# Performance work log

Hardware: AMD Instinct MI355X
Metric: run time of the kernel (lower is better)

The kernel has to match this reference:

```python
import jax, jax.numpy as jnp
import numpy as np

B, L, C_IN, H, W = 4, 5, 64, 256, 128
QUERY_SIZE, KEY_SIZE = 32, 256


def _conv_relu(x, w, b, stride):
    # conv2DBatchNormRelu with BN (eval) folded into conv weights/bias
    y = jax.lax.conv_general_dilated(x, w, (stride, stride), [(1, 1), (1, 1)],
                                     dimension_numbers=('NCHW', 'OIHW', 'NCHW'))
    return jax.nn.relu(y + b[None, :, None, None])


def _policy_net(x, w1, b1, w2, b2, w3, b3):
    # policy_net4: three stride-2 4x4 conv blocks -> (N, 64, H/8, W/8)
    x = _conv_relu(x, w1, b1, 2)
    x = _conv_relu(x, w2, b2, 2)
    return _conv_relu(x, w3, b3, 2)


def _km_generator(feat, f1w, f1b, f2w, f2b, f3w, f3b):
    # km_generator_v2: global avg pool + MLP 64->256->128->out_size
    x = feat.mean(axis=(2, 3))
    x = jax.nn.relu(x @ f1w.T + f1b)
    x = jax.nn.relu(x @ f2w.T + f2b)
    return x @ f3w.T + f3b


def _affine_grid(theta, h, w):
    # torch F.affine_grid, align_corners=False
    xs = (jnp.arange(w, dtype=jnp.float32) + 0.5) * (2.0 / w) - 1.0
    ys = (jnp.arange(h, dtype=jnp.float32) + 0.5) * (2.0 / h) - 1.0
    gy, gx = jnp.meshgrid(ys, xs, indexing='ij')
    base = jnp.stack([gx, gy, jnp.ones_like(gx)], axis=-1)  # (h, w, 3)
    return jnp.einsum('nij,hwj->nhwi', theta, base)  # (N, h, w, 2)


def _grid_sample(img, grid):
    # torch F.grid_sample, bilinear, padding_mode='zeros', align_corners=False
    n, c, h, w = img.shape
    x = ((grid[..., 0] + 1.0) * w - 1.0) * 0.5
    y = ((grid[..., 1] + 1.0) * h - 1.0) * 0.5
    x0, y0 = jnp.floor(x), jnp.floor(y)

    def gather(ix, iy):
        valid = (ix >= 0) & (ix < w) & (iy >= 0) & (iy < h)
        ixc = jnp.clip(ix, 0, w - 1).astype(jnp.int32)
        iyc = jnp.clip(iy, 0, h - 1).astype(jnp.int32)
        vals = jax.vmap(lambda im, yy, xx: im[:, yy, xx])(img, iyc, ixc)  # (n, c, h, w)
        return vals * valid[:, None, :, :].astype(img.dtype)

    wx1 = (x - x0)[:, None]
    wx0 = 1.0 - wx1
    wy1 = (y - y0)[:, None]
    wy0 = 1.0 - wy1
    return (gather(x0, y0) * wx0 * wy0 + gather(x0 + 1.0, y0) * wx1 * wy0 +
            gather(x0, y0 + 1.0) * wx0 * wy1 + gather(x0 + 1.0, y0 + 1.0) * wx1 * wy1)


def setup_inputs() -> dict:
    key = jax.random.key(0)
    ks = jax.random.split(key, 24)
    s = 0.05
    eye = jnp.array([[1.0, 0.0, 0.0], [0.0, 1.0, 0.0]], jnp.float32)
    nam = jnp.broadcast_to(eye, (B, L, L, 2, 3)) + s * jax.random.normal(ks[1], (B, L, L, 2, 3), jnp.float32)
    return {
        'x': jax.random.normal(ks[0], (B * L, C_IN, H, W), jnp.float32),
        'record_len': jnp.full((B,), L, jnp.int32),
        'normalized_affine_matrix': nam,
        'conv_w1': s * jax.random.normal(ks[2], (32, C_IN, 4, 4), jnp.float32),
        'conv_b1': jnp.zeros((32,), jnp.float32),
        'conv_w2': s * jax.random.normal(ks[3], (64, 32, 4, 4), jnp.float32),
        'conv_b2': jnp.zeros((64,), jnp.float32),
        'conv_w3': s * jax.random.normal(ks[4], (64, 64, 4, 4), jnp.float32),
        'conv_b3': jnp.zeros((64,), jnp.float32),
        'key_f1w': s * jax.random.normal(ks[5], (256, 64), jnp.float32),
        'key_f1b': jnp.zeros((256,), jnp.float32),
        'key_f2w': s * jax.random.normal(ks[6], (128, 256), jnp.float32),
        'key_f2b': jnp.zeros((128,), jnp.float32),
        'key_f3w': s * jax.random.normal(ks[7], (KEY_SIZE, 128), jnp.float32),
        'key_f3b': jnp.zeros((KEY_SIZE,), jnp.float32),
        'qry_f1w': s * jax.random.normal(ks[8], (256, 64), jnp.float32),
        'qry_f1b': jnp.zeros((256,), jnp.float32),
        'qry_f2w': s * jax.random.normal(ks[9], (128, 256), jnp.float32),
        'qry_f2b': jnp.zeros((128,), jnp.float32),
        'qry_f3w': s * jax.random.normal(ks[10], (QUERY_SIZE, 128), jnp.float32),
        'qry_f3b': jnp.zeros((QUERY_SIZE,), jnp.float32),
        'attn_w': s * jax.random.normal(ks[11], (KEY_SIZE, QUERY_SIZE), jnp.float32),
        'attn_b': jnp.zeros((KEY_SIZE,), jnp.float32),
    }


def reference(x, record_len, normalized_affine_matrix,
              conv_w1, conv_b1, conv_w2, conv_b2, conv_w3, conv_b3,
              key_f1w, key_f1b, key_f2w, key_f2b, key_f3w, key_f3b,
              qry_f1w, qry_f1b, qry_f2w, qry_f2b, qry_f3w, qry_f3b,
              attn_w, attn_b):
    # record_len is constant (= L for every sample) -> static regroup as reshape
    xb = x.reshape(B, L, C_IN, H, W)
    tmats = normalized_affine_matrix[:, 0]  # t_matrix[0]: warp every cav to ego, (B, L, 2, 3)

    def fuse_one(xi, ti):
        neigh = _grid_sample(xi, _affine_grid(ti, H, W))  # (L, C, H, W)
        maps = _policy_net(neigh, conv_w1, conv_b1, conv_w2, conv_b2, conv_w3, conv_b3)
        keys = _km_generator(maps, key_f1w, key_f1b, key_f2w, key_f2b, key_f3w, key_f3b)  # (L, KEY)
        qry = _km_generator(maps[:1], qry_f1w, qry_f1b, qry_f2w, qry_f2b, qry_f3w, qry_f3b)  # (1, QUERY)
        q = qry @ attn_w.T + attn_b  # (1, KEY)
        attn = jax.nn.softmax(keys @ q[0])  # softmax over key/agent axis, (L,)
        return jnp.einsum('n,nchw->chw', attn, neigh)

    return jax.vmap(fuse_one)(xb, tmats)  # (B, C, H, W)
```

## Files before the change

### kernel.cpp

```cpp
#include <hip/hip_runtime.h>
#include <hip/hip_bf16.h>

typedef __attribute__((ext_vector_type(8))) short short8;
typedef __attribute__((ext_vector_type(8))) unsigned short ushort8;
typedef __attribute__((ext_vector_type(4))) float floatx4;

static __device__ __forceinline__ float bf2f(unsigned short h) {
    unsigned int u = ((unsigned int)h) << 16;
    float f;
    __builtin_memcpy(&f, &u, 4);
    return f;
}
static __device__ __forceinline__ unsigned short f2bf(float f) {
    unsigned int u;
    __builtin_memcpy(&u, &f, 4);
    u = (u + 0x7FFFu + ((u >> 16) & 1u)) >> 16;
    return (unsigned short)u;
}

#define P_NAM 0
#define P_B1 600
#define P_B2 632
#define P_B3 696
#define P_K1W 760
#define P_K1B 17144
#define P_K2W 17400
#define P_K2B 50168
#define P_K3W 50296
#define P_K3B 83064
#define P_Q1W 83320
#define P_Q1B 99704
#define P_Q2W 99960
#define P_Q2B 132728
#define P_Q3W 132856
#define P_Q3B 136952
#define P_AW 136984
#define P_AB 145176
#define P_TOTAL 145432

__global__ void k_detect(const unsigned short* __restrict__ x, int* __restrict__ flag) {
    const int lane = threadIdx.x;
    const unsigned short h = x[2 * lane];
    const int e = (h >> 7) & 0xFF;
    const int ok = (e >= 110 && e <= 140) ? 1 : 0;
    unsigned long long m = __ballot(ok);
    if (lane == 0) *flag = (__popcll(m) >= 48) ? 0 : 1;
}

struct ParamDesc {
    const void* src[18];
    int len[18];
    int dst[18];
};

__global__ __launch_bounds__(256) void k_convert(ParamDesc pd, const int* __restrict__ flag,
                                                 float* __restrict__ out) {
    int idx = blockIdx.x * 256 + threadIdx.x;
    const int isf = *flag;
    for (int t = 0; t < 18; ++t) {
        const int l = pd.len[t];
        if (idx < l) {
            float v = isf ? ((const float*)pd.src[t])[idx]
                          : bf2f(((const unsigned short*)pd.src[t])[idx]);
            out[pd.dst[t] + idx] = v;
            return;
        }
        idx -= l;
    }
}

__global__ __launch_bounds__(256) void k_pack(
    const void* __restrict__ w1, const void* __restrict__ w2, const void* __restrict__ w3,
    const int* __restrict__ flag, short* __restrict__ blobs)
{
    const int idx = blockIdx.x * 256 + threadIdx.x;
    const int isf = *flag;
    if (idx < 32768) {
        int j = idx & 7, lane = (idx >> 3) & 63, t = (idx >> 9) & 1,
            s = (idx >> 10) & 3, c = (idx >> 12) & 1, ky = (idx >> 13) & 3;
        int kp = s * 32 + (lane >> 4) * 8 + j;
        int kx = kp >> 5, ic = c * 32 + (kp & 31), oc = t * 16 + (lane & 15);
        int si = oc * 1024 + ic * 16 + ky * 4 + kx;
        float v = isf ? ((const float*)w1)[si] : bf2f(((const unsigned short*)w1)[si]);
        blobs[idx] = (short)f2bf(v);
    } else if (idx < 65536) {
        int i2 = idx - 32768;
        int j = i2 & 7, lane = (i2 >> 3) & 63, t = (i2 >> 9) & 3,
            s = (i2 >> 11) & 3, ky = (i2 >> 13) & 3;
        int kp = s * 32 + (lane >> 4) * 8 + j;
        int kx = kp >> 5, ic = kp & 31, oc = t * 16 + (lane & 15);
        int si = oc * 512 + ic * 16 + ky * 4 + kx;
        float v = isf ? ((const float*)w2)[si] : bf2f(((const unsigned short*)w2)[si]);
        blobs[idx] = (short)f2bf(v);
    } else if (idx < 131072) {
        int i3 = idx - 65536;
        int j = i3 & 7, lane = (i3 >> 3) & 63, t = (i3 >> 9) & 3,
            s = (i3 >> 11) & 3, c = (i3 >> 13) & 1, ky = (i3 >> 14) & 3;
        int kp = s * 32 + (lane >> 4) * 8 + j;
        int kx = kp >> 5, ic = c * 32 + (kp & 31), oc = t * 16 + (lane & 15);
        int si = oc * 1024 + ic * 16 + ky * 4 + kx;
        float v = isf ? ((const float*)w3)[si] : bf2f(((const unsigned short*)w3)[si]);
        blobs[idx] = (short)f2bf(v);
    }
}

__global__ __launch_bounds__(128) void k_gridsample(
    const void* __restrict__ xv,
    const float* __restrict__ P,
    const int* __restrict__ flag,
    unsigned short* __restrict__ neighCL)
{
    __shared__ unsigned int s_t32[128 * 33];
    unsigned short* s_t = (unsigned short*)s_t32;
    const int n = blockIdx.x;
    const int h = blockIdx.y;
    const int w = threadIdx.x;
    const int b = n / 5, l = n - b * 5;
    const float* th = P + P_NAM + (b * 25 + l) * 6;
    const float t00 = th[0], t01 = th[1], t02 = th[2];
    const float t10 = th[3], t11 = th[4], t12 = th[5];

    const float gxn = ((float)w + 0.5f) * (2.0f / 128.0f) - 1.0f;
    const float gyn = ((float)h + 0.5f) * (2.0f / 256.0f) - 1.0f;
    const float gx = t00 * gxn + t01 * gyn + t02;
    const float gy = t10 * gxn + t11 * gyn + t12;
    const float xs = ((gx + 1.0f) * 128.0f - 1.0f) * 0.5f;
    const float ys = ((gy + 1.0f) * 256.0f - 1.0f) * 0.5f;
    const float x0f = floorf(xs), y0f = floorf(ys);
    const int ix0 = (int)x0f, iy0 = (int)y0f;
    const int ix1 = ix0 + 1, iy1 = iy0 + 1;
    const float wx1 = xs - x0f, wx0 = 1.0f - wx1;
    const float wy1 = ys - y0f, wy0 = 1.0f - wy1;

    const float mx0 = (ix0 >= 0 && ix0 < 128) ? 1.0f : 0.0f;
    const float mx1 = (ix1 >= 0 && ix1 < 128) ? 1.0f : 0.0f;
    const float my0 = (iy0 >= 0 && iy0 < 256) ? 1.0f : 0.0f;
    const float my1 = (iy1 >= 0 && iy1 < 256) ? 1.0f : 0.0f;
    const int cx0 = min(max(ix0, 0), 127), cx1 = min(max(ix1, 0), 127);
    const int cy0 = min(max(iy0, 0), 255), cy1 = min(max(iy1, 0), 255);

    const float w00 = mx0 * my0 * wx0 * wy0, w10 = mx1 * my0 * wx1 * wy0;
    const float w01 = mx0 * my1 * wx0 * wy1, w11 = mx1 * my1 * wx1 * wy1;
    const int o00 = cy0 * 128 + cx0, o10 = cy0 * 128 + cx1;
    const int o01 = cy1 * 128 + cx0, o11 = cy1 * 128 + cx1;

    if (*flag) {
        const float* img = ((const float*)xv) + (size_t)n * 64 * 32768;
        for (int c = 0; c < 64; ++c) {
            const float* ic = img + c * 32768;
            const float r = ic[o00] * w00 + ic[o10] * w10 + ic[o01] * w01 + ic[o11] * w11;
            s_t[w * 66 + c] = f2bf(r);
        }
    } else {
        const unsigned short* img = ((const unsigned short*)xv) + (size_t)n * 64 * 32768;
        for (int c = 0; c < 64; ++c) {
            const unsigned short* ic = img + c * 32768;
            const float r = bf2f(ic[o00]) * w00 + bf2f(ic[o10]) * w10 +
                            bf2f(ic[o01]) * w01 + bf2f(ic[o11]) * w11;
            s_t[w * 66 + c] = f2bf(r);
        }
    }
    __syncthreads();
    unsigned int* gout = (unsigned int*)(neighCL + ((size_t)n * 32768 + (size_t)h * 128) * 64);
    for (int e = w; e < 4096; e += 128) {
        const int px = e >> 5, part = e & 31;
        gout[px * 32 + part] = s_t32[px * 33 + part];
    }
}

#define ROWSTR 1096

__global__ __launch_bounds__(128) void k_conv1m(
    const unsigned short* __restrict__ in, const short* __restrict__ blob1,
    const float* __restrict__ P, unsigned short* __restrict__ out)
{
    __shared__ unsigned short s_a[18 * ROWSTR];
    __shared__ float sb[32];
    const int n = blockIdx.x;
    const int oy0 = blockIdx.y * 8;
    const int ox0 = blockIdx.z * 16;
    const int tid = threadIdx.x;
    const int wv = tid >> 6, lane = tid & 63;
    const int ln = lane & 15, q = lane >> 4;
    const int mrow = ln >> 2, mcol = ln & 3;
    const int iny0 = 2 * oy0 - 1, inx0 = 2 * ox0 - 1;
    if (tid < 32) sb[tid] = P[P_B1 + tid];

    floatx4 acc[4][2];
#pragma unroll
    for (int f = 0; f < 4; ++f)
#pragma unroll
        for (int t = 0; t < 2; ++t) acc[f][t] = (floatx4)0.0f;

    const ushort8 z8 = (ushort8)0;
    for (int c = 0; c < 2; ++c) {
        __syncthreads();
        for (int e = tid; e < 2448; e += 128) {
            const int row = e / 136, rem = e - row * 136;
            const int col = rem >> 2, part = rem & 3;
            const int gy = iny0 + row, gxp = inx0 + col;
            ushort8 v = z8;
            if (gy >= 0 && gy < 256 && gxp >= 0 && gxp < 128)
                v = *(const ushort8*)(in + (((size_t)n * 32768 + gy * 128 + gxp) * 64 + c * 32 + part * 8));
            *(ushort8*)(s_a + row * ROWSTR + col * 32 + part * 8) = v;
        }
        __syncthreads();
#pragma unroll
        for (int ky = 0; ky < 4; ++ky) {
            short8 bfr[4][2];
            const short* bb = blob1 + ((ky * 2 + c) * 8) * 512 + lane * 8;
#pragma unroll
            for (int s = 0; s < 4; ++s)
#pragma unroll
                for (int t = 0; t < 2; ++t)
                    bfr[s][t] = *(const short8*)(bb + (s * 2 + t) * 512);
#pragma unroll
            for (int f = 0; f < 4; ++f) {
                const int base = (2 * ((f >> 1) * 4 + mrow) + ky) * ROWSTR +
                                 (wv * 8 + (f & 1) * 4 + mcol) * 64 + q * 8;
#pragma unroll
                for (int s = 0; s < 4; ++s) {
                    const short8 a = *(const short8*)(s_a + base + s * 32);
#pragma unroll
                    for (int t = 0; t < 2; ++t)
                        acc[f][t] = __builtin_amdgcn_mfma_f32_16x16x32_bf16(a, bfr[s][t], acc[f][t], 0, 0, 0);
                }
            }
        }
    }
#pragma unroll
    for (int f = 0; f < 4; ++f)
#pragma unroll
        for (int t = 0; t < 2; ++t)
#pragma unroll
            for (int r = 0; r < 4; ++r) {
                const int oc = t * 16 + ln;
                const int oy = oy0 + (f >> 1) * 4 + q;
                const int ox = ox0 + wv * 8 + (f & 1) * 4 + r;
                float v = acc[f][t][r] + sb[oc];
                v = v > 0.0f ? v : 0.0f;
                out[(((size_t)n * 128 + oy) * 64 + ox) * 32 + oc] = f2bf(v);
            }
}

__global__ __launch_bounds__(256) void k_conv2m(
    const unsigned short* __restrict__ in, const short* __restrict__ blob2,
    const float* __restrict__ P, unsigned short* __restrict__ out)
{
    __shared__ unsigned short s_a[18 * ROWSTR];
    __shared__ float sb[64];
    const int n = blockIdx.x;
    const int oy0 = blockIdx.y * 8;
    const int ox0 = blockIdx.z * 16;
    const int tid = threadIdx.x;
    const int wave = tid >> 6, lane = tid & 63;
    const int wcol = wave & 1, wt = wave >> 1;
    const int ln = lane & 15, q = lane >> 4;
    const int mrow = ln >> 2, mcol = ln & 3;
    const int iny0 = 2 * oy0 - 1, inx0 = 2 * ox0 - 1;
    if (tid < 64) sb[tid] = P[P_B2 + tid];

    floatx4 acc[4][2];
#pragma unroll
    for (int f = 0; f < 4; ++f)
#pragma unroll
        for (int t = 0; t < 2; ++t) acc[f][t] = (floatx4)0.0f;

    const ushort8 z8 = (ushort8)0;
    for (int e = tid; e < 2448; e += 256) {
        const int row = e / 136, rem = e - row * 136;
        const int col = rem >> 2, part = rem & 3;
        const int gy = iny0 + row, gxp = inx0 + col;
        ushort8 v = z8;
        if (gy >= 0 && gy < 128 && gxp >= 0 && gxp < 64)
            v = *(const ushort8*)(in + (((size_t)n * 8192 + gy * 64 + gxp) * 32 + part * 8));
        *(ushort8*)(s_a + row * ROWSTR + col * 32 + part * 8) = v;
    }
    __syncthreads();
#pragma unroll
    for (int ky = 0; ky < 4; ++ky) {
        short8 bfr[4][2];
#pragma unroll
        for (int s = 0; s < 4; ++s)
#pragma unroll
            for (int tt = 0; tt < 2; ++tt)
                bfr[s][tt] = *(const short8*)(blob2 + ((ky * 4 + s) * 4 + wt * 2 + tt) * 512 + lane * 8);
#pragma unroll
        for (int f = 0; f < 4; ++f) {
            const int base = (2 * ((f >> 1) * 4 + mrow) + ky) * ROWSTR +
                             (wcol * 8 + (f & 1) * 4 + mcol) * 64 + q * 8;
#pragma unroll
            for (int s = 0; s < 4; ++s) {
                const short8 a = *(const short8*)(s_a + base + s * 32);
#pragma unroll
                for (int tt = 0; tt < 2; ++tt)
                    acc[f][tt] = __builtin_amdgcn_mfma_f32_16x16x32_bf16(a, bfr[s][tt], acc[f][tt], 0, 0, 0);
            }
        }
    }
#pragma unroll
    for (int f = 0; f < 4; ++f)
#pragma unroll
        for (int tt = 0; tt < 2; ++tt)
#pragma unroll
            for (int r = 0; r < 4; ++r) {
                const int oc = (wt * 2 + tt) * 16 + ln;
                const int oy = oy0 + (f >> 1) * 4 + q;
                const int ox = ox0 + wcol * 8 + (f & 1) * 4 + r;
                float v = acc[f][tt][r] + sb[oc];
                v = v > 0.0f ? v : 0.0f;
                out[(((size_t)n * 64 + oy) * 32 + ox) * 64 + oc] = f2bf(v);
            }
}

__global__ __launch_bounds__(256) void k_conv3m(
    const unsigned short* __restrict__ in, const short* __restrict__ blob3,
    const float* __restrict__ P, float* __restrict__ pooled)
{
    __shared__ unsigned short s_a[18 * ROWSTR];
    __shared__ float sb[64];
    const int n = blockIdx.x;
    const int oy0 = blockIdx.y * 8;
    const int tid = threadIdx.x;
    const int wave = tid >> 6, lane = tid & 63;
    const int wcol = wave & 1, wt = wave >> 1;
    const int ln = lane & 15, q = lane >> 4;
    const int mrow = ln >> 2, mcol = ln & 3;
    const int iny0 = 2 * oy0 - 1, inx0 = -1;
    if (tid < 64) sb[tid] = P[P_B3 + tid];

    floatx4 acc[4][2];
#pragma unroll
    for (int f = 0; f < 4; ++f)
#pragma unroll
        for (int t = 0; t < 2; ++t) acc[f][t] = (floatx4)0.0f;

    const ushort8 z8 = (ushort8)0;
    for (int c = 0; c < 2; ++c) {
        __syncthreads();
        for (int e = tid; e < 2448; e += 256) {
            const int row = e / 136, rem = e - row * 136;
            const int col = rem >> 2, part = rem & 3;
            const int gy = iny0 + row, gxp = inx0 + col;
            ushort8 v = z8;
            if (gy >= 0 && gy < 64 && gxp >= 0 && gxp < 32)
                v = *(const ushort8*)(in + (((size_t)n * 2048 + gy * 32 + gxp) * 64 + c * 32 + part * 8));
            *(ushort8*)(s_a + row * ROWSTR + col * 32 + part * 8) = v;
        }
        __syncthreads();
#pragma unroll
        for (int ky = 0; ky < 4; ++ky) {
            short8 bfr[4][2];
#pragma unroll
            for (int s = 0; s < 4; ++s)
#pragma unroll
                for (int tt = 0; tt < 2; ++tt)
                    bfr[s][tt] = *(const short8*)(blob3 + (((ky * 2 + c) * 4 + s) * 4 + wt * 2 + tt) * 512 + lane * 8);
#pragma unroll
            for (int f = 0; f < 4; ++f) {
                const int base = (2 * ((f >> 1) * 4 + mrow) + ky) * ROWSTR +
                                 (wcol * 8 + (f & 1) * 4 + mcol) * 64 + q * 8;
#pragma unroll
                for (int s = 0; s < 4; ++s) {
                    const short8 a = *(const short8*)(s_a + base + s * 32);
#pragma unroll
                    for (int tt = 0; tt < 2; ++tt)
                        acc[f][tt] = __builtin_amdgcn_mfma_f32_16x16x32_bf16(a, bfr[s][tt], acc[f][tt], 0, 0, 0);
                }
            }
        }
    }
#pragma unroll
    for (int tt = 0; tt < 2; ++tt) {
        const int oc = (wt * 2 + tt) * 16 + ln;
        float ps = 0.0f;
#pragma unroll
        for (int f = 0; f < 4; ++f)
#pragma unroll
            for (int r = 0; r < 4; ++r) {
                float v = acc[f][tt][r] + sb[oc];
                ps += (v > 0.0f ? v : 0.0f);
            }
        ps += __shfl_xor(ps, 16, 64);
        ps += __shfl_xor(ps, 32, 64);
        if (lane < 16) atomicAdd(&pooled[n * 64 + oc], ps);
    }
}

__global__ __launch_bounds__(256) void k_attn(
    const float* __restrict__ P,
    const float* __restrict__ pooled,
    float* __restrict__ attn)
{
    __shared__ float sfeat[320], sh1[1280], sh2[640], skeys[1280];
    __shared__ float sq1[256], sq2[128], sq3[32], sqv[256], sred[4], slog[5];
    const int b = blockIdx.x, t = threadIdx.x;

    for (int i = t; i < 320; i += 256) sfeat[i] = pooled[b * 320 + i] * (1.0f / 512.0f);
    __syncthreads();

    {
        const float* w = P + P_K1W; const float* bb = P + P_K1B;
        for (int l = 0; l < 5; ++l) {
            float s = bb[t];
            for (int c = 0; c < 64; ++c) s += w[t * 64 + c] * sfeat[l * 64 + c];
            sh1[l * 256 + t] = fmaxf(s, 0.0f);
        }
        const float* wq = P + P_Q1W; const float* bq = P + P_Q1B;
        float s = bq[t];
        for (int c = 0; c < 64; ++c) s += wq[t * 64 + c] * sfeat[c];
        sq1[t] = fmaxf(s, 0.0f);
    }
    __syncthreads();
    if (t < 128) {
        const float* w = P + P_K2W; const float* bb = P + P_K2B;
        for (int l = 0; l < 5; ++l) {
            float s = bb[t];
            for (int k = 0; k < 256; ++k) s += w[t * 256 + k] * sh1[l * 256 + k];
            sh2[l * 128 + t] = fmaxf(s, 0.0f);
        }
        const float* wq = P + P_Q2W; const float* bq = P + P_Q2B;
        float s = bq[t];
        for (int k = 0; k < 256; ++k) s += wq[t * 256 + k] * sq1[k];
        sq2[t] = fmaxf(s, 0.0f);
    }
    __syncthreads();
    {
        const float* w = P + P_K3W; const float* bb = P + P_K3B;
        for (int l = 0; l < 5; ++l) {
            float s = bb[t];
            for (int k = 0; k < 128; ++k) s += w[t * 128 + k] * sh2[l * 128 + k];
            skeys[l * 256 + t] = s;
        }
    }
    if (t < 32) {
        const float* wq = P + P_Q3W; const float* bq = P + P_Q3B;
        float s = bq[t];
        for (int k = 0; k < 128; ++k) s += wq[t * 128 + k] * sq2[k];
        sq3[t] = s;
    }
    __syncthreads();
    {
        const float* w = P + P_AW; const float* bb = P + P_AB;
        float s = bb[t];
        for (int k = 0; k < 32; ++k) s += w[t * 32 + k] * sq3[k];
        sqv[t] = s;
    }
    __syncthreads();
    for (int l = 0; l < 5; ++l) {
        float v = skeys[l * 256 + t] * sqv[t];
        for (int off = 32; off > 0; off >>= 1) v += __shfl_down(v, off, 64);
        if ((t & 63) == 0) sred[t >> 6] = v;
        __syncthreads();
        if (t == 0) slog[l] = sred[0] + sred[1] + sred[2] + sred[3];
        __syncthreads();
    }
    if (t == 0) {
        float m = slog[0];
        for (int l = 1; l < 5; ++l) m = fmaxf(m, slog[l]);
        float e[5], s = 0.0f;
        for (int l = 0; l < 5; ++l) { e[l] = expf(slog[l] - m); s += e[l]; }
        const float inv = 1.0f / s;
        for (int l = 0; l < 5; ++l) attn[b * 5 + l] = e[l] * inv;
    }
}

__global__ __launch_bounds__(256) void k_final(
    const unsigned short* __restrict__ neighCL,
    const float* __restrict__ attn,
    float* __restrict__ out)
{
    const int blk = blockIdx.x;
    const int b = blk >> 9;
    const int px0 = (blk & 511) << 6;
    const int t = threadIdx.x;
    const int p = t >> 2, part = t & 3;
    const float* a = attn + b * 5;
    float acc[16];
#pragma unroll
    for (int i = 0; i < 16; ++i) acc[i] = 0.0f;
#pragma unroll
    for (int l = 0; l < 5; ++l) {
        const ushort8* src = (const ushort8*)(neighCL +
            (((size_t)(b * 5 + l) * 32768 + px0 + p) * 64 + part * 16));
        const ushort8 v0 = src[0], v1 = src[1];
        const float wl = a[l];
#pragma unroll
        for (int j = 0; j < 8; ++j) {
            acc[j]     += wl * bf2f(v0[j]);
            acc[8 + j] += wl * bf2f(v1[j]);
        }
    }
#pragma unroll
    for (int ch = 0; ch < 2; ++ch)
#pragma unroll
        for (int j = 0; j < 8; ++j) {
            const int c = part * 16 + ch * 8 + j;
            out[((size_t)b * 64 + c) * 32768 + px0 + p] = acc[ch * 8 + j];
        }
}

extern "C" void kernel_launch(void* const* d_in, const int* in_sizes, int n_in,
                              void* d_out, int out_size, void* d_ws, size_t ws_size,
                              hipStream_t stream) {
    const size_t OFF_FLAG  = 0;
    const size_t OFF_PARAM = 256;
    const size_t OFF_BLOB  = 582016;
    const size_t OFF_NEIGH = 844160;
    const size_t OFF_C1    = OFF_NEIGH + 83886080;
    const size_t OFF_C2    = OFF_C1 + 10485760;
    const size_t OFF_POOL  = OFF_C2 + 5242880;
    const size_t OFF_ATTN  = OFF_POOL + 5120;
    const size_t NEED      = OFF_ATTN + 80;
    if (ws_size < NEED) return;

    char* ws = (char*)d_ws;
    int*   flag   = (int*)(ws + OFF_FLAG);
    float* params = (float*)(ws + OFF_PARAM);
    short* blobs  = (short*)(ws + OFF_BLOB);
    unsigned short* neighCL = (unsigned short*)(ws + OFF_NEIGH);
    unsigned short* c1      = (unsigned short*)(ws + OFF_C1);
    unsigned short* c2      = (unsigned short*)(ws + OFF_C2);
    float* pooled           = (float*)(ws + OFF_POOL);
    float* attn             = (float*)(ws + OFF_ATTN);

    ParamDesc pd;
    const int srcIdx[18] = {2,4,6,8,9,10,11,12,13,14,15,16,17,18,19,20,21,22};
    const int lens[18]   = {600,32,64,64,16384,256,32768,128,32768,256,
                            16384,256,32768,128,4096,32,8192,256};
    const int dsts[18]   = {P_NAM,P_B1,P_B2,P_B3,P_K1W,P_K1B,P_K2W,P_K2B,P_K3W,P_K3B,
                            P_Q1W,P_Q1B,P_Q2W,P_Q2B,P_Q3W,P_Q3B,P_AW,P_AB};
    for (int t = 0; t < 18; ++t) {
        pd.src[t] = d_in[srcIdx[t]];
        pd.len[t] = lens[t];
        pd.dst[t] = dsts[t];
    }

    hipMemsetAsync(pooled, 0, 5120, stream);

    k_detect<<<1, 64, 0, stream>>>((const unsigned short*)d_in[0], flag);
    k_convert<<<569, 256, 0, stream>>>(pd, flag, params);
    k_pack<<<512, 256, 0, stream>>>(d_in[3], d_in[5], d_in[7], flag, blobs);
    k_gridsample<<<dim3(20, 256), 128, 0, stream>>>(d_in[0], params, flag, neighCL);
    k_conv1m<<<dim3(20, 16, 4), 128, 0, stream>>>(neighCL, blobs, params, c1);
    k_conv2m<<<dim3(20, 8, 2), 256, 0, stream>>>(c1, blobs + 32768, params, c2);
    k_conv3m<<<dim3(20, 4, 1), 256, 0, stream>>>(c2, blobs + 65536, params, pooled);
    k_attn<<<4, 256, 0, stream>>>(params, pooled, attn);
    k_final<<<2048, 256, 0, stream>>>(neighCL, attn, (float*)d_out);
}
```

Measured before the change: 521.1 us.

## Fuse prep kernels, inline dtype detection, and write gridsample output directly

Merges the detect, convert and pack kernels into one prep kernel, and each kernel now detects the input dtype itself with a wave ballot instead of reading a flag from memory. Grid sample now handles two rows per 256-thread block and writes each pixel's 64 channels as 16-byte vector stores straight to global memory, dropping the shared-memory transpose and its barrier. This removes two launches and an LDS round trip. The price is per-block redundant detection loads, and the per-thread stores are strided by 128 bytes across lanes instead of coalesced through LDS.

```diff
diff --git a/kernel.cpp b/kernel.cpp
--- a/kernel.cpp
+++ b/kernel.cpp
@@ -16,6 +16,15 @@
     __builtin_memcpy(&u, &f, 4);
     u = (u + 0x7FFFu + ((u >> 16) & 1u)) >> 16;
     return (unsigned short)u;
+}
+
+static __device__ __forceinline__ int detect_f32(const void* xv) {
+    const unsigned short* xu = (const unsigned short*)xv;
+    const int lane = threadIdx.x & 63;
+    const unsigned short h = xu[2 * lane];
+    const int e = (h >> 7) & 0xFF;
+    unsigned long long m = __ballot(e >= 110 && e <= 140);
+    return (__popcll(m) >= 48) ? 0 : 1;
 }
 
 #define P_NAM 0
@@ -38,43 +47,19 @@
 #define P_AB 145176
 #define P_TOTAL 145432
 
-__global__ void k_detect(const unsigned short* __restrict__ x, int* __restrict__ flag) {
-    const int lane = threadIdx.x;
-    const unsigned short h = x[2 * lane];
-    const int e = (h >> 7) & 0xFF;
-    const int ok = (e >= 110 && e <= 140) ? 1 : 0;
-    unsigned long long m = __ballot(ok);
-    if (lane == 0) *flag = (__popcll(m) >= 48) ? 0 : 1;
-}
-
 struct ParamDesc {
     const void* src[18];
     int len[18];
     int dst[18];
 };
 
-__global__ __launch_bounds__(256) void k_convert(ParamDesc pd, const int* __restrict__ flag,
-                                                 float* __restrict__ out) {
+__global__ __launch_bounds__(256) void k_prep(
+    const void* __restrict__ xv,
+    const void* __restrict__ w1, const void* __restrict__ w2, const void* __restrict__ w3,
+    ParamDesc pd, short* __restrict__ blobs, float* __restrict__ params)
+{
+    const int isf = detect_f32(xv);
     int idx = blockIdx.x * 256 + threadIdx.x;
-    const int isf = *flag;
-    for (int t = 0; t < 18; ++t) {
-        const int l = pd.len[t];
-        if (idx < l) {
-            float v = isf ? ((const float*)pd.src[t])[idx]
-                          : bf2f(((const unsigned short*)pd.src[t])[idx]);
-            out[pd.dst[t] + idx] = v;
-            return;
-        }
-        idx -= l;
-    }
-}
-
-__global__ __launch_bounds__(256) void k_pack(
-    const void* __restrict__ w1, const void* __restrict__ w2, const void* __restrict__ w3,
-    const int* __restrict__ flag, short* __restrict__ blobs)
-{
-    const int idx = blockIdx.x * 256 + threadIdx.x;
-    const int isf = *flag;
     if (idx < 32768) {
         int j = idx & 7, lane = (idx >> 3) & 63, t = (idx >> 9) & 1,
             s = (idx >> 10) & 3, c = (idx >> 12) & 1, ky = (idx >> 13) & 3;
@@ -83,6 +68,7 @@
         int si = oc * 1024 + ic * 16 + ky * 4 + kx;
         float v = isf ? ((const float*)w1)[si] : bf2f(((const unsigned short*)w1)[si]);
         blobs[idx] = (short)f2bf(v);
+        return;
     } else if (idx < 65536) {
         int i2 = idx - 32768;
         int j = i2 & 7, lane = (i2 >> 3) & 63, t = (i2 >> 9) & 3,
@@ -92,6 +78,7 @@
         int si = oc * 512 + ic * 16 + ky * 4 + kx;
         float v = isf ? ((const float*)w2)[si] : bf2f(((const unsigned short*)w2)[si]);
         blobs[idx] = (short)f2bf(v);
+        return;
     } else if (idx < 131072) {
         int i3 = idx - 65536;
         int j = i3 & 7, lane = (i3 >> 3) & 63, t = (i3 >> 9) & 3,
@@ -101,20 +88,30 @@
         int si = oc * 1024 + ic * 16 + ky * 4 + kx;
         float v = isf ? ((const float*)w3)[si] : bf2f(((const unsigned short*)w3)[si]);
         blobs[idx] = (short)f2bf(v);
-    }
-}
-
-__global__ __launch_bounds__(128) void k_gridsample(
+        return;
+    }
+    idx -= 131072;
+    for (int t = 0; t < 18; ++t) {
+        const int l = pd.len[t];
+        if (idx < l) {
+            float v = isf ? ((const float*)pd.src[t])[idx]
+                          : bf2f(((const unsigned short*)pd.src[t])[idx]);
+            params[pd.dst[t] + idx] = v;
+            return;
+        }
+        idx -= l;
+    }
+}
+
+__global__ __launch_bounds__(256) void k_gridsample(
     const void* __restrict__ xv,
     const float* __restrict__ P,
-    const int* __restrict__ flag,
     unsigned short* __restrict__ neighCL)
 {
-    __shared__ unsigned int s_t32[128 * 33];
-    unsigned short* s_t = (unsigned short*)s_t32;
+    const int isf = detect_f32(xv);
     const int n = blockIdx.x;
-    const int h = blockIdx.y;
-    const int w = threadIdx.x;
+    const int h = blockIdx.y * 2 + (threadIdx.x >> 7);
+    const int w = threadIdx.x & 127;
     const int b = n / 5, l = n - b * 5;
     const float* th = P + P_NAM + (b * 25 + l) * 6;
     const float t00 = th[0], t01 = th[1], t02 = th[2];
@@ -144,27 +141,46 @@
     const int o00 = cy0 * 128 + cx0, o10 = cy0 * 128 + cx1;
     const int o01 = cy1 * 128 + cx0, o11 = cy1 * 128 + cx1;
 
-    if (*flag) {
-        const float* img = ((const float*)xv) + (size_t)n * 64 * 32768;
-        for (int c = 0; c < 64; ++c) {
-            const float* ic = img + c * 32768;
-            const float r = ic[o00] * w00 + ic[o10] * w10 + ic[o01] * w01 + ic[o11] * w11;
-            s_t[w * 66 + c] = f2bf(r);
+    unsigned short* outp = neighCL + ((size_t)n * 32768 + (size_t)h * 128 + w) * 64;
+    if (isf) {
+        const float* img = ((const float*)xv) + (size_t)n * 2097152;
+        const float* p00 = img + o00; const float* p10 = img + o10;
+        const float* p01 = img + o01; const float* p11 = img + o11;
+#pragma unroll
+        for (int c0 = 0; c0 < 64; c0 += 8) {
+            float v00[8], v10[8], v01[8], v11[8];
+#pragma unroll
+            for (int j = 0; j < 8; ++j) {
+                const int off = (c0 + j) * 32768;
+                v00[j] = p00[off]; v10[j] = p10[off];
+                v01[j] = p01[off]; v11[j] = p11[off];
+            }
+            ushort8 r;
+#pragma unroll
+            for (int j = 0; j < 8; ++j)
+                r[j] = f2bf(v00[j] * w00 + v10[j] * w10 + v01[j] * w01 + v11[j] * w11);
+            *(ushort8*)(outp + c0) = r;
         }
     } else {
-        const unsigned short* img = ((const unsigned short*)xv) + (size_t)n * 64 * 32768;
-        for (int c = 0; c < 64; ++c) {
-            const unsigned short* ic = img + c * 32768;
-            const float r = bf2f(ic[o00]) * w00 + bf2f(ic[o10]) * w10 +
-                            bf2f(ic[o01]) * w01 + bf2f(ic[o11]) * w11;
-            s_t[w * 66 + c] = f2bf(r);
-        }
-    }
-    __syncthreads();
-    unsigned int* gout = (unsigned int*)(neighCL + ((size_t)n * 32768 + (size_t)h * 128) * 64);
-    for (int e = w; e < 4096; e += 128) {
-        const int px = e >> 5, part = e & 31;
-        gout[px * 32 + part] = s_t32[px * 33 + part];
+        const unsigned short* img = ((const unsigned short*)xv) + (size_t)n * 2097152;
+        const unsigned short* p00 = img + o00; const unsigned short* p10 = img + o10;
+        const unsigned short* p01 = img + o01; const unsigned short* p11 = img + o11;
+#pragma unroll
+        for (int c0 = 0; c0 < 64; c0 += 8) {
+            unsigned short v00[8], v10[8], v01[8], v11[8];
+#pragma unroll
+            for (int j = 0; j < 8; ++j) {
+                const int off = (c0 + j) * 32768;
+                v00[j] = p00[off]; v10[j] = p10[off];
+                v01[j] = p01[off]; v11[j] = p11[off];
+            }
+            ushort8 r;
+#pragma unroll
+            for (int j = 0; j < 8; ++j)
+                r[j] = f2bf(bf2f(v00[j]) * w00 + bf2f(v10[j]) * w10 +
+                            bf2f(v01[j]) * w01 + bf2f(v11[j]) * w11);
+            *(ushort8*)(outp + c0) = r;
+        }
     }
 }
 
@@ -503,10 +519,9 @@
 extern "C" void kernel_launch(void* const* d_in, const int* in_sizes, int n_in,
                               void* d_out, int out_size, void* d_ws, size_t ws_size,
                               hipStream_t stream) {
-    const size_t OFF_FLAG  = 0;
-    const size_t OFF_PARAM = 256;
-    const size_t OFF_BLOB  = 582016;
-    const size_t OFF_NEIGH = 844160;
+    const size_t OFF_PARAM = 0;
+    const size_t OFF_BLOB  = 581760;
+    const size_t OFF_NEIGH = 843904;
     const size_t OFF_C1    = OFF_NEIGH + 83886080;
     const size_t OFF_C2    = OFF_C1 + 10485760;
     const size_t OFF_POOL  = OFF_C2 + 5242880;
@@ -515,7 +530,6 @@
     if (ws_size < NEED) return;
 
     char* ws = (char*)d_ws;
-    int*   flag   = (int*)(ws + OFF_FLAG);
     float* params = (float*)(ws + OFF_PARAM);
     short* blobs  = (short*)(ws + OFF_BLOB);
     unsigned short* neighCL = (unsigned short*)(ws + OFF_NEIGH);
@@ -538,10 +552,8 @@
 
     hipMemsetAsync(pooled, 0, 5120, stream);
 
-    k_detect<<<1, 64, 0, stream>>>((const unsigned short*)d_in[0], flag);
-    k_convert<<<569, 256, 0, stream>>>(pd, flag, params);
-    k_pack<<<512, 256, 0, stream>>>(d_in[3], d_in[5], d_in[7], flag, blobs);
-    k_gridsample<<<dim3(20, 256), 128, 0, stream>>>(d_in[0], params, flag, neighCL);
+    k_prep<<<1081, 256, 0, stream>>>(d_in[0], d_in[3], d_in[5], d_in[7], pd, blobs, params);
+    k_gridsample<<<dim3(20, 128), 256, 0, stream>>>(d_in[0], params, neighCL);
     k_conv1m<<<dim3(20, 16, 4), 128, 0, stream>>>(neighCL, blobs, params, c1);
     k_conv2m<<<dim3(20, 8, 2), 256, 0, stream>>>(c1, blobs + 32768, params, c2);
     k_conv3m<<<dim3(20, 4, 1), 256, 0, stream>>>(c2, blobs + 65536, params, pooled);
```

New measurement: 621.1 us. +19.2%, slower.
